# Kernel optimization log

Measured on AMD Instinct MI355X. Metric: run time of the kernel, lower is better.

## Reference

```python
import jax, jax.numpy as jnp
import numpy as np

E, D, H, K = 8, 2048, 1024, 2  # num_experts, input_size, hidden_size, top_k
B, L = 2, 1024


def setup_inputs() -> dict:
    key = jax.random.key(0)
    k1, k2, k3, k4 = jax.random.split(key, 4)
    x = jax.random.normal(k1, (B, L, D), dtype=jnp.float32)
    w_gate = jax.random.normal(k2, (E, D), dtype=jnp.float32) * 0.02   # router Linear weight [E, D]
    w_in = jax.random.normal(k3, (E, 2 * H, D), dtype=jnp.float32) * 0.02  # ParallelExperts [E, out=2H, in=D]
    w_out = jax.random.normal(k4, (E, D, H), dtype=jnp.float32) * 0.02     # ParallelExperts [E, out=D, in=H]
    bias = jnp.zeros((D,), dtype=jnp.float32)
    return {"x": x, "w_gate": w_gate, "w_in": w_in, "w_out": w_out, "bias": bias}


def _moe_forward(x, w_gate, w_in, w_out, bias):
    bsz, length, d = x.shape
    xt = x.reshape(-1, d)  # [T, D]
    # top-k router: logits -> top-k -> softmax over selected logits
    logits = xt @ w_gate.T  # [T, E]
    topk_vals, topk_idx = jax.lax.top_k(logits, K)  # [T, K]
    topk_gates = jax.nn.softmax(topk_vals, axis=-1)  # [T, K]
    T = xt.shape[0]
    # dense [T, E] gate matrix; zero for non-selected experts, so the dense
    # per-expert compute below is mathematically identical to gathered dispatch
    gates = jnp.zeros((T, E), dtype=xt.dtype).at[jnp.arange(T)[:, None], topk_idx].add(topk_gates)
    # expert GLU FFN, vectorized over experts
    h = jnp.einsum('td,efd->tef', xt, w_in)  # [T, E, 2H]
    h1, h2 = jnp.split(h, 2, axis=-1)
    a = jax.nn.silu(h1) * h2                 # [T, E, H]
    eo = jnp.einsum('teh,edh->ted', a, w_out)  # [T, E, D]
    y = jnp.einsum('ted,te->td', eo, gates) + bias
    return y.reshape(bsz, length, d)


def reference(x, w_gate, w_in, w_out, bias):
    y = _moe_forward(x, w_gate, w_in, w_out, bias)
    loss = jnp.float32(0.0)  # router aux loss is 0 in eval mode (JetMoE top_k_gating)
    return (y, loss)
```

## Files before the change

kernel.cpp:

```cpp
#include <hip/hip_runtime.h>
#include <hip/hip_bf16.h>

#define E_    8
#define D_    2048
#define H_    1024
#define T_    2048
#define BK    64

using u16   = unsigned short;
using s16x8 = __attribute__((ext_vector_type(8))) short;
using f32x4 = __attribute__((ext_vector_type(4))) float;

#define WAITVM(N) asm volatile("s_waitcnt vmcnt(" #N ")" ::: "memory")
#define LGKM0     asm volatile("s_waitcnt lgkmcnt(0)" ::: "memory")
#define SB0       __builtin_amdgcn_sched_barrier(0)

__device__ __forceinline__ short f2bf(float f) {
  __hip_bfloat16 h = __float2bfloat16(f);
  return __builtin_bit_cast(short, h);
}
__device__ __forceinline__ s16x8 cvt8(f32x4 a, f32x4 b) {
  s16x8 o;
  o[0]=f2bf(a.x); o[1]=f2bf(a.y); o[2]=f2bf(a.z); o[3]=f2bf(a.w);
  o[4]=f2bf(b.x); o[5]=f2bf(b.y); o[6]=f2bf(b.z); o[7]=f2bf(b.w);
  return o;
}
__device__ __forceinline__ int slot(int r, int c) { return r * 64 + ((c ^ (r & 7)) << 3); }

__device__ __forceinline__ void gload16(const void* g, void* l) {
  __builtin_amdgcn_global_load_lds((const __attribute__((address_space(1))) void*)g,
                                   (__attribute__((address_space(3))) void*)l, 16, 0, 0);
}

#define FIND_EXPERT(ml, cnt, e, mt, Ne, RND, SH)               \
  { int b_ = 0;                                                \
    _Pragma("unroll")                                          \
    for (int i_ = 0; i_ < E_; ++i_) {                          \
      int ti_ = (cnt[i_] + RND) >> SH;                         \
      if ((ml) >= b_ && (ml) < b_ + ti_) {                     \
        e = i_; mt = (ml) - b_; Ne = cnt[i_]; }                \
      b_ += ti_; } }


__global__ __launch_bounds__(256) void init_kernel(
    const float* __restrict__ bias, float* __restrict__ out, int* __restrict__ counts)
{
  int idx = blockIdx.x * 256 + threadIdx.x;
  if (blockIdx.x == 0 && threadIdx.x < E_) counts[threadIdx.x] = 0;
  if (idx == 0) out[(size_t)T_ * D_] = 0.0f;
  int dq = idx & (D_ / 4 - 1);
  f32x4 b = *(const f32x4*)(bias + dq * 4);
  *(f32x4*)(out + (size_t)idx * 4) = b;
}

__global__ __launch_bounds__(256) void router_kernel(
    const float* __restrict__ x, const float* __restrict__ wg,
    u16* __restrict__ xb, int* __restrict__ lists, float* __restrict__ gates,
    int* __restrict__ counts)
{
  int t = blockIdx.x;
  int tid = threadIdx.x;
  const float* xr = x + (size_t)t * D_;
  float acc[E_];
#pragma unroll
  for (int e = 0; e < E_; ++e) acc[e] = 0.f;
#pragma unroll
  for (int i = 0; i < D_ / 256; ++i) {
    int d = tid + 256 * i;
    float xv = xr[d];
    xb[(size_t)t * D_ + d] = (u16)f2bf(xv);
#pragma unroll
    for (int e = 0; e < E_; ++e) acc[e] += xv * wg[e * D_ + d];
  }
#pragma unroll
  for (int off = 32; off >= 1; off >>= 1)
#pragma unroll
    for (int e = 0; e < E_; ++e) acc[e] += __shfl_down(acc[e], off);

  __shared__ float red[4][E_];
  int w = tid >> 6, lane = tid & 63;
  if (lane == 0)
#pragma unroll
    for (int e = 0; e < E_; ++e) red[w][e] = acc[e];
  __syncthreads();
  if (tid == 0) {
    float v0 = -1e30f, v1 = -1e30f; int e0 = 0, e1 = 0;
#pragma unroll
    for (int e = 0; e < E_; ++e) {
      float v = red[0][e] + red[1][e] + red[2][e] + red[3][e];
      if (v > v0)      { v1 = v0; e1 = e0; v0 = v; e0 = e; }
      else if (v > v1) { v1 = v;  e1 = e; }
    }
    float g1 = expf(v1 - v0);
    float inv = 1.f / (1.f + g1);
    float g0 = inv; g1 *= inv;
    int s0 = atomicAdd(&counts[e0], 1);
    lists[e0 * T_ + s0] = t * 2 + 0;
    gates[t * 2 + 0] = g0;
    int s1 = atomicAdd(&counts[e1], 1);
    lists[e1 * T_ + s1] = t * 2 + 1;
    gates[t * 2 + 1] = g1;
  }
}

__global__ __launch_bounds__(512, 1) void gemm1_kernel(
    const u16* __restrict__ xb, const float* __restrict__ w_in,
    const int* __restrict__ lists, const int* __restrict__ counts,
    u16* __restrict__ a_buf)
{
  __shared__ __align__(16) u16 As[3][256 * 64];
  __shared__ __align__(16) u16 Bs[2][128 * 64];

  int cnt[E_];
#pragma unroll
  for (int i = 0; i < E_; ++i) cnt[i] = counts[i];
  int mt_total = 0;
#pragma unroll
  for (int i = 0; i < E_; ++i) mt_total += (cnt[i] + 255) >> 8;
  int total = mt_total * 16;
  int chunk = (total + 7) >> 3;

  int tid = threadIdx.x, w = tid >> 6, lane = tid & 63;
  int swzc = ((lane & 7) ^ (lane >> 3)) * 8;
  int brow = tid >> 2, bc = (tid & 3) * 2;
  int wr = (w >> 2) * 128, wc = (w & 3) * 32, lrow = lane & 15, g = lane >> 4;
  int lcol = lane & 15, lr4 = (lane >> 4) * 4;
  int xcd = blockIdx.x & 7, bslot = blockIdx.x >> 3;

  for (int sl = bslot; sl < chunk; sl += 32) {
    int t = xcd * chunk + sl;
    if (t >= total) break;
    int ml = t >> 4, n = t & 15;
    int e = 0, mt = 0, Ne = 0;
    FIND_EXPERT(ml, cnt, e, mt, Ne, 255, 8);

    const u16* ap[4];
#pragma unroll
    for (int i = 0; i < 4; ++i) {
      int gr = mt * 256 + 32 * w + 8 * i + (lane >> 3);
      if (gr >= Ne) gr = Ne - 1;
      ap[i] = xb + (size_t)(lists[e * T_ + gr] >> 1) * D_ + swzc;
    }
    int o = n * 64 + ((brow >> 4) & 1) * H_ + (brow >> 5) * 16 + (brow & 15);
    const float* bp = w_in + (size_t)e * (2 * H_) * D_ + (size_t)o * D_ + bc * 8;

    f32x4 acc[8][2];
#pragma unroll
    for (int m = 0; m < 8; ++m) { acc[m][0] = (f32x4){0,0,0,0}; acc[m][1] = (f32x4){0,0,0,0}; }
    f32x4 bl[4];

#pragma unroll
    for (int j = 0; j < 4; ++j) bl[j] = *(const f32x4*)(bp + j * 4);
    SB0;
#pragma unroll
    for (int i = 0; i < 4; ++i) gload16(ap[i], &As[0][(32 * w + 8 * i) * 64]);
    SB0;
#pragma unroll
    for (int i = 0; i < 4; ++i) gload16(ap[i] + BK, &As[1][(32 * w + 8 * i) * 64]);
    SB0;
    WAITVM(8);  SB0;
    *(s16x8*)(&Bs[0][slot(brow, bc)])     = cvt8(bl[0], bl[1]);
    *(s16x8*)(&Bs[0][slot(brow, bc + 1)]) = cvt8(bl[2], bl[3]);
    SB0;
#pragma unroll
    for (int j = 0; j < 4; ++j) bl[j] = *(const f32x4*)(bp + BK + j * 4);
    SB0;
    WAITVM(8);  SB0;
    LGKM0;
    __builtin_amdgcn_s_barrier();

    const int NT = D_ / BK;
    for (int kt = 0; kt < NT; ++kt) {
      int cur = kt % 3;
      if (kt + 2 < NT) {
        int wrt = cur + 2; if (wrt >= 3) wrt -= 3;
        int k2 = (kt + 2) * BK;
        SB0;
#pragma unroll
        for (int i = 0; i < 4; ++i) gload16(ap[i] + k2, &As[wrt][(32 * w + 8 * i) * 64]);
        SB0;
      }
#pragma unroll
      for (int ks = 0; ks < 2; ++ks) {
        int ch = ks * 4 + g;
        s16x8 af[8], bf[2];
#pragma unroll
        for (int m = 0; m < 8; ++m) af[m] = *(const s16x8*)(&As[cur][slot(wr + m * 16 + lrow, ch)]);
        bf[0] = *(const s16x8*)(&Bs[kt & 1][slot(wc + lrow, ch)]);
        bf[1] = *(const s16x8*)(&Bs[kt & 1][slot(wc + 16 + lrow, ch)]);
        __builtin_amdgcn_s_setprio(1);
#pragma unroll
        for (int m = 0; m < 8; ++m)
#pragma unroll
          for (int nn = 0; nn < 2; ++nn)
            acc[m][nn] = __builtin_amdgcn_mfma_f32_16x16x32_bf16(af[m], bf[nn], acc[m][nn], 0, 0, 0);
        __builtin_amdgcn_s_setprio(0);
      }
      if (kt + 1 < NT) {
        if (kt + 2 < NT) { WAITVM(4); } else { WAITVM(0); }
        SB0;
        *(s16x8*)(&Bs[(kt + 1) & 1][slot(brow, bc)])     = cvt8(bl[0], bl[1]);
        *(s16x8*)(&Bs[(kt + 1) & 1][slot(brow, bc + 1)]) = cvt8(bl[2], bl[3]);
        SB0;
        if (kt + 2 < NT) {
          int k2 = (kt + 2) * BK;
#pragma unroll
          for (int j = 0; j < 4; ++j) bl[j] = *(const f32x4*)(bp + k2 + j * 4);
          SB0;
        }
        LGKM0;
        __builtin_amdgcn_s_barrier();
      }
    }
    LGKM0;
    __builtin_amdgcn_s_barrier();
#pragma unroll
    for (int m = 0; m < 8; ++m)
#pragma unroll
      for (int q = 0; q < 4; ++q) {
        int row = mt * 256 + wr + m * 16 + lr4 + q;
        if (row < Ne) {
          float h1 = acc[m][0][q], h2 = acc[m][1][q];
          float a = (h1 / (1.f + __expf(-h1))) * h2;
          a_buf[((size_t)e * T_ + row) * H_ + n * 64 + (w & 3) * 16 + lcol] = (u16)f2bf(a);
        }
      }
  }
}

__global__ __launch_bounds__(512, 2) void gemm2_kernel(
    const u16* __restrict__ a_buf, const float* __restrict__ w_out,
    const int* __restrict__ lists, const int* __restrict__ counts,
    const float* __restrict__ gates, float* __restrict__ out)
{
  __shared__ __align__(16) u16 As[3][128 * 64];
  __shared__ __align__(16) u16 Bs[2][128 * 64];

  int cnt[E_];
#pragma unroll
  for (int i = 0; i < E_; ++i) cnt[i] = counts[i];
  int mt_total = 0;
#pragma unroll
  for (int i = 0; i < E_; ++i) mt_total += (cnt[i] + 127) >> 7;
  int total = mt_total * 16;
  int chunk = (total + 7) >> 3;

  int tid = threadIdx.x, w = tid >> 6, lane = tid & 63;
  int swzc = ((lane & 7) ^ (lane >> 3)) * 8;
  int brow = tid >> 2, bc = (tid & 3) * 2;
  int wr = (w >> 2) * 64, wc = (w & 3) * 32, lrow = lane & 15, g = lane >> 4;
  int lcol = lane & 15, lr4 = (lane >> 4) * 4;
  int xcd = blockIdx.x & 7, bslot = blockIdx.x >> 3;

  for (int sl = bslot; sl < chunk; sl += 64) {
    int t = xcd * chunk + sl;
    if (t >= total) break;
    int ml = t >> 4, n = t & 15;
    int e = 0, mt = 0, Ne = 0;
    FIND_EXPERT(ml, cnt, e, mt, Ne, 127, 7);

    const u16* ap[2];
#pragma unroll
    for (int i = 0; i < 2; ++i) {
      int gr = mt * 128 + 16 * w + 8 * i + (lane >> 3);
      if (gr >= Ne) gr = Ne - 1;
      ap[i] = a_buf + ((size_t)e * T_ + gr) * H_ + swzc;
    }
    const float* bp = w_out + (size_t)e * D_ * H_ + (size_t)(n * 128 + brow) * H_ + bc * 8;

    f32x4 acc[4][2];
#pragma unroll
    for (int m = 0; m < 4; ++m) { acc[m][0] = (f32x4){0,0,0,0}; acc[m][1] = (f32x4){0,0,0,0}; }
    f32x4 bl[4];

#pragma unroll
    for (int j = 0; j < 4; ++j) bl[j] = *(const f32x4*)(bp + j * 4);
    SB0;
#pragma unroll
    for (int i = 0; i < 2; ++i) gload16(ap[i], &As[0][(16 * w + 8 * i) * 64]);
    SB0;
#pragma unroll
    for (int i = 0; i < 2; ++i) gload16(ap[i] + BK, &As[1][(16 * w + 8 * i) * 64]);
    SB0;
    WAITVM(4);  SB0;
    *(s16x8*)(&Bs[0][slot(brow, bc)])     = cvt8(bl[0], bl[1]);
    *(s16x8*)(&Bs[0][slot(brow, bc + 1)]) = cvt8(bl[2], bl[3]);
    SB0;
#pragma unroll
    for (int j = 0; j < 4; ++j) bl[j] = *(const f32x4*)(bp + BK + j * 4);
    SB0;
    WAITVM(6);  SB0;
    LGKM0;
    __builtin_amdgcn_s_barrier();

    const int NT = H_ / BK;
    for (int kt = 0; kt < NT; ++kt) {
      int cur = kt % 3;
      if (kt + 2 < NT) {
        int wrt = cur + 2; if (wrt >= 3) wrt -= 3;
        int k2 = (kt + 2) * BK;
        SB0;
#pragma unroll
        for (int i = 0; i < 2; ++i) gload16(ap[i] + k2, &As[wrt][(16 * w + 8 * i) * 64]);
        SB0;
      }
#pragma unroll
      for (int ks = 0; ks < 2; ++ks) {
        int ch = ks * 4 + g;
        s16x8 af[4], bf[2];
#pragma unroll
        for (int m = 0; m < 4; ++m) af[m] = *(const s16x8*)(&As[cur][slot(wr + m * 16 + lrow, ch)]);
        bf[0] = *(const s16x8*)(&Bs[kt & 1][slot(wc + lrow, ch)]);
        bf[1] = *(const s16x8*)(&Bs[kt & 1][slot(wc + 16 + lrow, ch)]);
        __builtin_amdgcn_s_setprio(1);
#pragma unroll
        for (int m = 0; m < 4; ++m)
#pragma unroll
          for (int nn = 0; nn < 2; ++nn)
            acc[m][nn] = __builtin_amdgcn_mfma_f32_16x16x32_bf16(af[m], bf[nn], acc[m][nn], 0, 0, 0);
        __builtin_amdgcn_s_setprio(0);
      }
      if (kt + 1 < NT) {
        if (kt + 2 < NT) { WAITVM(2); } else { WAITVM(0); }
        SB0;
        *(s16x8*)(&Bs[(kt + 1) & 1][slot(brow, bc)])     = cvt8(bl[0], bl[1]);
        *(s16x8*)(&Bs[(kt + 1) & 1][slot(brow, bc + 1)]) = cvt8(bl[2], bl[3]);
        SB0;
        if (kt + 2 < NT) {
          int k2 = (kt + 2) * BK;
#pragma unroll
          for (int j = 0; j < 4; ++j) bl[j] = *(const f32x4*)(bp + k2 + j * 4);
          SB0;
        }
        LGKM0;
        __builtin_amdgcn_s_barrier();
      }
    }
    LGKM0;
    __builtin_amdgcn_s_barrier();
#pragma unroll
    for (int m = 0; m < 4; ++m)
#pragma unroll
      for (int q = 0; q < 4; ++q) {
        int row = mt * 128 + wr + m * 16 + lr4 + q;
        if (row < Ne) {
          int p = lists[e * T_ + row];
          float gt = gates[p];
          int tok = p >> 1;
#pragma unroll
          for (int nn = 0; nn < 2; ++nn)
            atomicAdd(&out[(size_t)tok * D_ + n * 128 + wc + nn * 16 + lcol], gt * acc[m][nn][q]);
        }
      }
  }
}

extern "C" void kernel_launch(void* const* d_in, const int* in_sizes, int n_in,
                              void* d_out, int out_size, void* d_ws, size_t ws_size,
                              hipStream_t stream)
{
  const float* x      = (const float*)d_in[0];
  const float* w_gate = (const float*)d_in[1];
  const float* w_in   = (const float*)d_in[2];
  const float* w_out  = (const float*)d_in[3];
  const float* bias   = (const float*)d_in[4];
  float* out = (float*)d_out;

  char* ws = (char*)d_ws;
  u16*   xb     = (u16*)(ws);
  u16*   a_buf  = (u16*)(ws + 8388608);
  int*   lists  = (int*)(ws + 41943040);
  float* gates  = (float*)(ws + 42008576);
  int*   counts = (int*)(ws + 42024960);

  init_kernel<<<T_ * D_ / 4 / 256, 256, 0, stream>>>(bias, out, counts);
  router_kernel<<<T_, 256, 0, stream>>>(x, w_gate, xb, lists, gates, counts);
  gemm1_kernel<<<256, 512, 0, stream>>>(xb, w_in, lists, counts, a_buf);
  gemm2_kernel<<<512, 512, 0, stream>>>(a_buf, w_out, lists, counts, gates, out);
}
```

Measured before the change: 231.7 us.

## Pre-convert w_out to bf16, simplify gemm2 pipeline, remap gemm1 tiles per XCD

Adds a pass that converts w_out from fp32 to bf16 into workspace so gemm2 can stream both operands directly into LDS with async loads. The gemm2 main loop becomes a plain double buffer that waits and syncs every k-step. Bias initialisation moves into the router kernel and counts are zeroed with a memset. gemm1 tile assignment is remapped so each XCD handles contiguous M tiles across all N tiles, which should improve L2 reuse of activations. The extra conversion pass reads and writes 64MB+32MB every call, and the full wait per k-step removes overlap in gemm2.

```diff
diff --git a/kernel.cpp b/kernel.cpp
--- a/kernel.cpp
+++ b/kernel.cpp
@@ -12,6 +12,7 @@
 using f32x4 = __attribute__((ext_vector_type(4))) float;
 
 #define WAITVM(N) asm volatile("s_waitcnt vmcnt(" #N ")" ::: "memory")
+#define WAITVM0   asm volatile("s_waitcnt vmcnt(0)" ::: "memory")
 #define LGKM0     asm volatile("s_waitcnt lgkmcnt(0)" ::: "memory")
 #define SB0       __builtin_amdgcn_sched_barrier(0)
 
@@ -42,24 +43,44 @@
       b_ += ti_; } }
 
 
-__global__ __launch_bounds__(256) void init_kernel(
-    const float* __restrict__ bias, float* __restrict__ out, int* __restrict__ counts)
-{
-  int idx = blockIdx.x * 256 + threadIdx.x;
-  if (blockIdx.x == 0 && threadIdx.x < E_) counts[threadIdx.x] = 0;
-  if (idx == 0) out[(size_t)T_ * D_] = 0.0f;
-  int dq = idx & (D_ / 4 - 1);
-  f32x4 b = *(const f32x4*)(bias + dq * 4);
-  *(f32x4*)(out + (size_t)idx * 4) = b;
+#define WOUT_ELEMS 16777216
+
+__global__ __launch_bounds__(256) void convert_kernel(
+    const float* __restrict__ src, u16* __restrict__ dst, int n)
+{
+  int stride = gridDim.x * 256 * 16;
+  for (int i = (blockIdx.x * 256 + threadIdx.x) * 16; i < n; i += stride) {
+    f32x4 a0 = *(const f32x4*)(src + i);
+    f32x4 a1 = *(const f32x4*)(src + i + 4);
+    f32x4 a2 = *(const f32x4*)(src + i + 8);
+    f32x4 a3 = *(const f32x4*)(src + i + 12);
+    s16x8 o0, o1;
+    o0[0]=f2bf(a0.x); o0[1]=f2bf(a0.y); o0[2]=f2bf(a0.z); o0[3]=f2bf(a0.w);
+    o0[4]=f2bf(a1.x); o0[5]=f2bf(a1.y); o0[6]=f2bf(a1.z); o0[7]=f2bf(a1.w);
+    o1[0]=f2bf(a2.x); o1[1]=f2bf(a2.y); o1[2]=f2bf(a2.z); o1[3]=f2bf(a2.w);
+    o1[4]=f2bf(a3.x); o1[5]=f2bf(a3.y); o1[6]=f2bf(a3.z); o1[7]=f2bf(a3.w);
+    *(s16x8*)(dst + i)     = o0;
+    *(s16x8*)(dst + i + 8) = o1;
+  }
 }
 
 __global__ __launch_bounds__(256) void router_kernel(
     const float* __restrict__ x, const float* __restrict__ wg,
+    const float* __restrict__ bias,
     u16* __restrict__ xb, int* __restrict__ lists, float* __restrict__ gates,
-    int* __restrict__ counts)
+    int* __restrict__ counts, float* __restrict__ out)
 {
   int t = blockIdx.x;
   int tid = threadIdx.x;
+
+  {
+    const float* bp = bias + tid * 8;
+    f32x4 b0 = *(const f32x4*)(bp), b1 = *(const f32x4*)(bp + 4);
+    *(f32x4*)(out + (size_t)t * D_ + tid * 8)     = b0;
+    *(f32x4*)(out + (size_t)t * D_ + tid * 8 + 4) = b1;
+    if (t == 0 && tid == 0) out[(size_t)T_ * D_] = 0.0f;
+  }
+
   const float* xr = x + (size_t)t * D_;
   float acc[E_];
 #pragma unroll
@@ -117,20 +138,29 @@
   int mt_total = 0;
 #pragma unroll
   for (int i = 0; i < E_; ++i) mt_total += (cnt[i] + 255) >> 8;
-  int total = mt_total * 16;
-  int chunk = (total + 7) >> 3;
+
+  int xcd = blockIdx.x & 7, bslot = blockIdx.x >> 3;
+  int mg = mt_total >> 3, rem = mt_total & 7;
+  int nbase = mg * 16;
+  int strays = rem * 16 > xcd ? (rem * 16 - xcd + 7) >> 3 : 0;
+  int mytiles = nbase + strays;
 
   int tid = threadIdx.x, w = tid >> 6, lane = tid & 63;
   int swzc = ((lane & 7) ^ (lane >> 3)) * 8;
   int brow = tid >> 2, bc = (tid & 3) * 2;
   int wr = (w >> 2) * 128, wc = (w & 3) * 32, lrow = lane & 15, g = lane >> 4;
   int lcol = lane & 15, lr4 = (lane >> 4) * 4;
-  int xcd = blockIdx.x & 7, bslot = blockIdx.x >> 3;
-
-  for (int sl = bslot; sl < chunk; sl += 32) {
-    int t = xcd * chunk + sl;
-    if (t >= total) break;
-    int ml = t >> 4, n = t & 15;
+
+  for (int li = bslot; li < mytiles; li += 32) {
+    int ml, n;
+    if (li < nbase) {
+      n = li / mg;
+      ml = xcd * mg + (li - n * mg);
+    } else {
+      int j = (li - nbase) * 8 + xcd;
+      ml = mg * 8 + (j >> 4);
+      n = j & 15;
+    }
     int e = 0, mt = 0, Ne = 0;
     FIND_EXPERT(ml, cnt, e, mt, Ne, 255, 8);
 
@@ -229,11 +259,11 @@
 }
 
 __global__ __launch_bounds__(512, 2) void gemm2_kernel(
-    const u16* __restrict__ a_buf, const float* __restrict__ w_out,
+    const u16* __restrict__ a_buf, const u16* __restrict__ wb_out,
     const int* __restrict__ lists, const int* __restrict__ counts,
     const float* __restrict__ gates, float* __restrict__ out)
 {
-  __shared__ __align__(16) u16 As[3][128 * 64];
+  __shared__ __align__(16) u16 As[2][128 * 64];
   __shared__ __align__(16) u16 Bs[2][128 * 64];
 
   int cnt[E_];
@@ -247,7 +277,6 @@
 
   int tid = threadIdx.x, w = tid >> 6, lane = tid & 63;
   int swzc = ((lane & 7) ^ (lane >> 3)) * 8;
-  int brow = tid >> 2, bc = (tid & 3) * 2;
   int wr = (w >> 2) * 64, wc = (w & 3) * 32, lrow = lane & 15, g = lane >> 4;
   int lcol = lane & 15, lr4 = (lane >> 4) * 4;
   int xcd = blockIdx.x & 7, bslot = blockIdx.x >> 3;
@@ -262,47 +291,39 @@
     const u16* ap[2];
 #pragma unroll
     for (int i = 0; i < 2; ++i) {
-      int gr = mt * 128 + 16 * w + 8 * i + (lane >> 3);
+      int gr = mt * 128 + w * 8 + i * 64 + (lane >> 3);
       if (gr >= Ne) gr = Ne - 1;
       ap[i] = a_buf + ((size_t)e * T_ + gr) * H_ + swzc;
     }
-    const float* bp = w_out + (size_t)e * D_ * H_ + (size_t)(n * 128 + brow) * H_ + bc * 8;
+    const u16* bp[2];
+#pragma unroll
+    for (int i = 0; i < 2; ++i) {
+      int br = w * 8 + i * 64 + (lane >> 3);
+      bp[i] = wb_out + (size_t)e * D_ * H_ + (size_t)(n * 128 + br) * H_ + swzc;
+    }
 
     f32x4 acc[4][2];
 #pragma unroll
     for (int m = 0; m < 4; ++m) { acc[m][0] = (f32x4){0,0,0,0}; acc[m][1] = (f32x4){0,0,0,0}; }
-    f32x4 bl[4];
-
-#pragma unroll
-    for (int j = 0; j < 4; ++j) bl[j] = *(const f32x4*)(bp + j * 4);
-    SB0;
-#pragma unroll
-    for (int i = 0; i < 2; ++i) gload16(ap[i], &As[0][(16 * w + 8 * i) * 64]);
-    SB0;
-#pragma unroll
-    for (int i = 0; i < 2; ++i) gload16(ap[i] + BK, &As[1][(16 * w + 8 * i) * 64]);
-    SB0;
-    WAITVM(4);  SB0;
-    *(s16x8*)(&Bs[0][slot(brow, bc)])     = cvt8(bl[0], bl[1]);
-    *(s16x8*)(&Bs[0][slot(brow, bc + 1)]) = cvt8(bl[2], bl[3]);
-    SB0;
-#pragma unroll
-    for (int j = 0; j < 4; ++j) bl[j] = *(const f32x4*)(bp + BK + j * 4);
-    SB0;
-    WAITVM(6);  SB0;
-    LGKM0;
-    __builtin_amdgcn_s_barrier();
+
+#pragma unroll
+    for (int i = 0; i < 2; ++i) {
+      gload16(ap[i], &As[0][(w * 8 + i * 64) * 64]);
+      gload16(bp[i], &Bs[0][(w * 8 + i * 64) * 64]);
+    }
+    WAITVM0;
+    __syncthreads();
 
     const int NT = H_ / BK;
     for (int kt = 0; kt < NT; ++kt) {
-      int cur = kt % 3;
-      if (kt + 2 < NT) {
-        int wrt = cur + 2; if (wrt >= 3) wrt -= 3;
-        int k2 = (kt + 2) * BK;
-        SB0;
-#pragma unroll
-        for (int i = 0; i < 2; ++i) gload16(ap[i] + k2, &As[wrt][(16 * w + 8 * i) * 64]);
-        SB0;
+      int cur = kt & 1;
+      if (kt + 1 < NT) {
+        int k = (kt + 1) * BK;
+#pragma unroll
+        for (int i = 0; i < 2; ++i) {
+          gload16(ap[i] + k, &As[cur ^ 1][(w * 8 + i * 64) * 64]);
+          gload16(bp[i] + k, &Bs[cur ^ 1][(w * 8 + i * 64) * 64]);
+        }
       }
 #pragma unroll
       for (int ks = 0; ks < 2; ++ks) {
@@ -310,34 +331,17 @@
         s16x8 af[4], bf[2];
 #pragma unroll
         for (int m = 0; m < 4; ++m) af[m] = *(const s16x8*)(&As[cur][slot(wr + m * 16 + lrow, ch)]);
-        bf[0] = *(const s16x8*)(&Bs[kt & 1][slot(wc + lrow, ch)]);
-        bf[1] = *(const s16x8*)(&Bs[kt & 1][slot(wc + 16 + lrow, ch)]);
-        __builtin_amdgcn_s_setprio(1);
+#pragma unroll
+        for (int s = 0; s < 2; ++s)  bf[s] = *(const s16x8*)(&Bs[cur][slot(wc + s * 16 + lrow, ch)]);
 #pragma unroll
         for (int m = 0; m < 4; ++m)
 #pragma unroll
-          for (int nn = 0; nn < 2; ++nn)
-            acc[m][nn] = __builtin_amdgcn_mfma_f32_16x16x32_bf16(af[m], bf[nn], acc[m][nn], 0, 0, 0);
-        __builtin_amdgcn_s_setprio(0);
-      }
-      if (kt + 1 < NT) {
-        if (kt + 2 < NT) { WAITVM(2); } else { WAITVM(0); }
-        SB0;
-        *(s16x8*)(&Bs[(kt + 1) & 1][slot(brow, bc)])     = cvt8(bl[0], bl[1]);
-        *(s16x8*)(&Bs[(kt + 1) & 1][slot(brow, bc + 1)]) = cvt8(bl[2], bl[3]);
-        SB0;
-        if (kt + 2 < NT) {
-          int k2 = (kt + 2) * BK;
-#pragma unroll
-          for (int j = 0; j < 4; ++j) bl[j] = *(const f32x4*)(bp + k2 + j * 4);
-          SB0;
-        }
-        LGKM0;
-        __builtin_amdgcn_s_barrier();
-      }
-    }
-    LGKM0;
-    __builtin_amdgcn_s_barrier();
+          for (int s = 0; s < 2; ++s)
+            acc[m][s] = __builtin_amdgcn_mfma_f32_16x16x32_bf16(af[m], bf[s], acc[m][s], 0, 0, 0);
+      }
+      WAITVM0;
+      __syncthreads();
+    }
 #pragma unroll
     for (int m = 0; m < 4; ++m)
 #pragma unroll
@@ -348,8 +352,8 @@
           float gt = gates[p];
           int tok = p >> 1;
 #pragma unroll
-          for (int nn = 0; nn < 2; ++nn)
-            atomicAdd(&out[(size_t)tok * D_ + n * 128 + wc + nn * 16 + lcol], gt * acc[m][nn][q]);
+          for (int s = 0; s < 2; ++s)
+            atomicAdd(&out[(size_t)tok * D_ + n * 128 + wc + s * 16 + lcol], gt * acc[m][s][q]);
         }
       }
   }
@@ -369,12 +373,14 @@
   char* ws = (char*)d_ws;
   u16*   xb     = (u16*)(ws);
   u16*   a_buf  = (u16*)(ws + 8388608);
-  int*   lists  = (int*)(ws + 41943040);
-  float* gates  = (float*)(ws + 42008576);
-  int*   counts = (int*)(ws + 42024960);
-
-  init_kernel<<<T_ * D_ / 4 / 256, 256, 0, stream>>>(bias, out, counts);
-  router_kernel<<<T_, 256, 0, stream>>>(x, w_gate, xb, lists, gates, counts);
+  u16*   wb_out = (u16*)(ws + 41943040);
+  int*   lists  = (int*)(ws + 75497472);
+  float* gates  = (float*)(ws + 75563008);
+  int*   counts = (int*)(ws + 75579392);
+
+  hipMemsetAsync(counts, 0, 32, stream);
+  convert_kernel<<<2048, 256, 0, stream>>>(w_out, wb_out, WOUT_ELEMS);
+  router_kernel<<<T_, 256, 0, stream>>>(x, w_gate, bias, xb, lists, gates, counts, out);
   gemm1_kernel<<<256, 512, 0, stream>>>(xb, w_in, lists, counts, a_buf);
-  gemm2_kernel<<<512, 512, 0, stream>>>(a_buf, w_out, lists, counts, gates, out);
-}
+  gemm2_kernel<<<512, 512, 0, stream>>>(a_buf, wb_out, lists, counts, gates, out);
+}
```

Measured after the change: 257.3 us. 11.1% more time.
